# Optimization experiments

Measured on AMD Instinct MI355X. Metric: run time of the kernel, lower is better.

Reference implementation:

```python
import jax, jax.numpy as jnp
import numpy as np

B, S, L = 2, 512, 12
DIM, H, HD = 1024, 16, 64
MAX_SEQ, DFF = 1024, 4096
VOCAB, CODE_HEADS = 2048, 7
THETA, EPS = 10000.0, 1e-5


def _rope_tables():
    inv_freq = 1.0 / (THETA ** (jnp.arange(0, HD, 2, dtype=jnp.float32) / HD))
    t = jnp.arange(MAX_SEQ, dtype=jnp.float32)
    freqs = t[:, None] * inv_freq[None, :]          # [MAX, HD/2]
    emb = jnp.concatenate([freqs, freqs], axis=-1)  # [MAX, HD]
    return jnp.cos(emb), jnp.sin(emb)


def _rotate_half(x):
    x1, x2 = x[..., : HD // 2], x[..., HD // 2:]
    return jnp.concatenate([-x2, x1], axis=-1)


def _rms(x, w):
    v = jnp.mean(x * x, axis=-1, keepdims=True)
    return x * jax.lax.rsqrt(v + EPS) * w


def setup_inputs() -> dict:
    key = jax.random.key(0)
    ks = jax.random.split(key, 12)
    std = 0.02
    rn = lambda k, shp: jax.random.normal(k, shp, jnp.float32) * std
    fused_input2 = jax.random.normal(ks[0], (B, S, DIM), jnp.float32)
    primary_hidden = jax.random.normal(ks[1], (B, S, DIM), jnp.float32)
    position_ids = jnp.broadcast_to(jnp.arange(S), (B, S))
    cache_position = jnp.arange(S)
    # causal additive mask over the full cache length
    allowed = jnp.arange(MAX_SEQ)[None, :] <= cache_position[:, None]  # [S, MAX]
    attn_mask = jnp.broadcast_to(
        jnp.where(allowed, 0.0, -1e9)[None, None], (B, 1, S, MAX_SEQ)
    ).astype(jnp.float32)
    return {
        'fused_input2': fused_input2,
        'primary_hidden': primary_hidden,
        'attn_mask': attn_mask,
        'w_bridge': rn(ks[2], (2 * DIM, DIM)),
        'ln1_w': jnp.ones((L, DIM), jnp.float32),
        'wq': rn(ks[3], (L, DIM, DIM)),
        'wk': rn(ks[4], (L, DIM, DIM)),
        'wv': rn(ks[5], (L, DIM, DIM)),
        'wo': rn(ks[6], (L, DIM, DIM)),
        'ln2_w': jnp.ones((L, DIM), jnp.float32),
        'w_gate': rn(ks[7], (L, DIM, DFF)),
        'w_up': rn(ks[8], (L, DIM, DFF)),
        'w_down': rn(ks[9], (L, DFF, DIM)),
        'norm_w': jnp.ones((DIM,), jnp.float32),
        'w_out': rn(ks[10], (CODE_HEADS, DIM, VOCAB)),
        'position_ids': position_ids,
        'cache_position': cache_position,
    }


def reference(fused_input2, primary_hidden, attn_mask, w_bridge, ln1_w, wq, wk, wv,
              wo, ln2_w, w_gate, w_up, w_down, norm_w, w_out,
              position_ids, cache_position):
    rope_cos, rope_sin = _rope_tables()
    cos = rope_cos[position_ids][:, None]  # [B,1,S,HD]
    sin = rope_sin[position_ids][:, None]
    scale = 1.0 / np.sqrt(HD).astype(np.float32)
    h = jnp.concatenate([fused_input2, primary_hidden], axis=-1) @ w_bridge
    for i in range(L):
        x = _rms(h, ln1_w[i])
        q = (x @ wq[i]).reshape(B, S, H, HD).transpose(0, 2, 1, 3)
        k = (x @ wk[i]).reshape(B, S, H, HD).transpose(0, 2, 1, 3)
        v = (x @ wv[i]).reshape(B, S, H, HD).transpose(0, 2, 1, 3)
        q = q * cos + _rotate_half(q) * sin
        k = k * cos + _rotate_half(k) * sin
        # scatter-style KV-cache write at cache_position
        kc = jnp.zeros((B, H, MAX_SEQ, HD), x.dtype).at[:, :, cache_position, :].set(k)
        vc = jnp.zeros((B, H, MAX_SEQ, HD), x.dtype).at[:, :, cache_position, :].set(v)
        s = jnp.einsum('bhsd,bhtd->bhst', q, kc) * scale + attn_mask
        p = jax.nn.softmax(s.astype(jnp.float32), axis=-1).astype(x.dtype)
        o = jnp.einsum('bhst,bhtd->bhsd', p, vc).transpose(0, 2, 1, 3).reshape(B, S, DIM)
        h = h + o @ wo[i]
        r = h
        x = _rms(h, ln2_w[i])
        h = r + (jax.nn.silu(x @ w_gate[i]) * (x @ w_up[i])) @ w_down[i]
    h = _rms(h, norm_w)
    # [B, code_depth-1, S, VOCAB]
    return jnp.einsum('bsd,kdv->bksv', h, w_out).astype(jnp.float32)
```

## Files before the change

kernel.cpp:

```cpp
#include <hip/hip_runtime.h>

#define NB    2
#define SEQ   512
#define NL    12
#define DIM   1024
#define NH    16
#define HD    64
#define DFF   4096
#define VOCAB 2048
#define CHD   7

typedef __attribute__((ext_vector_type(4))) float f32x4;
typedef __attribute__((ext_vector_type(8))) short s16x8;
typedef __attribute__((ext_vector_type(4))) unsigned short u16x4;
typedef __attribute__((ext_vector_type(8))) unsigned short u16x8;

__device__ __forceinline__ unsigned short f2bf(float f) {
    unsigned u = __builtin_bit_cast(unsigned, f);
    u += 0x7fffu + ((u >> 16) & 1u);
    return (unsigned short)(u >> 16);
}

__device__ __forceinline__ void gl2lds16(const void* g, void* l) {
    __builtin_amdgcn_global_load_lds(
        (const __attribute__((address_space(1))) void*)g,
        (__attribute__((address_space(3))) void*)l, 16, 0, 0);
}

template<int EPI>
__global__ __launch_bounds__(256)
void gemm_bf(const unsigned short* __restrict__ A,
             const unsigned short* __restrict__ B0,
             const unsigned short* __restrict__ B1,
             const unsigned short* __restrict__ B2,
             float* __restrict__ C, int K, int lda, int ldbT, int ldc,
             int rhi, long sBz, long sCz, int kchunk, int ksplit,
             const float* __restrict__ tc, const float* __restrict__ ts,
             const int* __restrict__ pid, unsigned short* __restrict__ qkv_bf)
{
    __shared__ unsigned short sm[4][8192];

    const int tid = threadIdx.x;
    const int z   = blockIdx.z;
    const int wsel = z / ksplit, kz = z - wsel * ksplit;
    const int m0  = blockIdx.y * 128;
    const int n0  = blockIdx.x * 128;
    const int koff = kz * kchunk;

    const unsigned short* Ap = A + koff;
    const unsigned short* Bp = sBz ? (B0 + (long)wsel * sBz)
                                   : (wsel == 0 ? B0 : (wsel == 1 ? B1 : B2));
    Bp += koff;
    float* Cp = C + (long)wsel * sCz;

    const int w = tid >> 6, l = tid & 63;
    const int lrow = l & 15, lhi = l >> 4;
    const int wm = (w >> 1) * 64, wn = (w & 1) * 64;

    int rowS[4], colS[4];
    #pragma unroll
    for (int i = 0; i < 4; ++i) {
        const int c = w * 256 + i * 64 + l;
        rowS[i] = c >> 3;
        colS[i] = (((c & 7) ^ ((c >> 3) & 7)) << 3);
    }

    f32x4 acc[4][4] = {};

    auto STAGE = [&](int d, int k0) {
        unsigned short* Ab = &sm[d * 2][0];
        unsigned short* Bb = &sm[d * 2 + 1][0];
        #pragma unroll
        for (int i = 0; i < 4; ++i) {
            const int ub = (w * 256 + i * 64) * 8;
            gl2lds16(Ap + (long)(m0 + rowS[i]) * lda + k0 + colS[i], Ab + ub);
            gl2lds16(Bp + (long)(n0 + rowS[i]) * ldbT + k0 + colS[i], Bb + ub);
        }
    };
    auto COMPUTE = [&](int d) {
        const char* Ab = (const char*)&sm[d * 2][0];
        const char* Bb = (const char*)&sm[d * 2 + 1][0];
        #pragma unroll
        for (int ks = 0; ks < 2; ++ks) {
            s16x8 af[4], bf[4];
            #pragma unroll
            for (int i = 0; i < 4; ++i) {
                const int r = wm + i * 16 + lrow;
                af[i] = __builtin_bit_cast(s16x8, *reinterpret_cast<const u16x8*>(
                    Ab + r * 128 + (((ks * 4 + lhi) ^ (r & 7)) << 4)));
            }
            #pragma unroll
            for (int j = 0; j < 4; ++j) {
                const int r = wn + j * 16 + lrow;
                bf[j] = __builtin_bit_cast(s16x8, *reinterpret_cast<const u16x8*>(
                    Bb + r * 128 + (((ks * 4 + lhi) ^ (r & 7)) << 4)));
            }
            #pragma unroll
            for (int i = 0; i < 4; ++i)
                #pragma unroll
                for (int j = 0; j < 4; ++j)
                    acc[i][j] = __builtin_amdgcn_mfma_f32_16x16x32_bf16(af[i], bf[j], acc[i][j], 0, 0, 0);
        }
    };

    STAGE(0, 0);
    __syncthreads();
    int cur = 0;
    for (int k0 = 0; k0 < K; k0 += 64) {
        if (k0 + 64 < K) STAGE(cur ^ 1, k0 + 64);
        COMPUTE(cur);
        __syncthreads();
        cur ^= 1;
    }

    if (EPI == 2) {
        const int h = (n0 + wn) >> 6;
        unsigned short* qb = qkv_bf;
        unsigned short* kb = qkv_bf + 1048576;
        unsigned short* vt = qkv_bf + 2097152;
        #pragma unroll
        for (int i = 0; i < 4; ++i) {
            const int r0 = m0 + wm + i * 16 + lhi * 4;
            #pragma unroll
            for (int e = 0; e < 4; ++e) {
                const int r = r0 + e;
                if (wsel == 2) {
                    const int bh = (r >> 9) * NH + h, s = r & 511;
                    #pragma unroll
                    for (int j = 0; j < 4; ++j)
                        vt[((long)(bh * 64 + j * 16 + lrow)) * 512 + s] = f2bf(acc[i][j][e]);
                } else {
                    unsigned short* ob = (wsel == 0) ? qb : kb;
                    const int pos = pid[r];
                    const float c0 = tc[pos * 32 + lrow],      s0 = ts[pos * 32 + lrow];
                    const float c1 = tc[pos * 32 + 16 + lrow], s1 = ts[pos * 32 + 16 + lrow];
                    const float a0 = acc[i][0][e], a1 = acc[i][1][e];
                    const float a2 = acc[i][2][e], a3 = acc[i][3][e];
                    const long rb = (long)r * DIM + (n0 + wn) + lrow;
                    ob[rb]      = f2bf(a0 * c0 - a2 * s0);
                    ob[rb + 16] = f2bf(a1 * c1 - a3 * s1);
                    ob[rb + 32] = f2bf(a2 * c0 + a0 * s0);
                    ob[rb + 48] = f2bf(a3 * c1 + a1 * s1);
                }
            }
        }
        return;
    }

    #pragma unroll
    for (int i = 0; i < 4; ++i) {
        const int r0 = m0 + wm + i * 16 + lhi * 4;
        #pragma unroll
        for (int j = 0; j < 4; ++j) {
            const int c = n0 + wn + j * 16 + lrow;
            #pragma unroll
            for (int e = 0; e < 4; ++e) {
                const int r = r0 + e;
                const long idx = (long)(r >> 9) * rhi + (long)(r & 511) * ldc + c;
                if (EPI == 1) atomicAdd(&Cp[idx], acc[i][j][e]);
                else          Cp[idx] = acc[i][j][e];
            }
        }
    }
}

__global__ __launch_bounds__(256)
void gemm_gu(const unsigned short* __restrict__ A,
             const unsigned short* __restrict__ Bg0,
             const unsigned short* __restrict__ Bu0,
             unsigned short* __restrict__ GU, int K, int lda, int ldbT)
{
    __shared__ unsigned short sm[32768];
    char* const lds = (char*)sm;

    const int tid = threadIdx.x;
    const int m0  = blockIdx.y * 128;
    const int n0  = blockIdx.x * 64;

    const unsigned short* Bg = Bg0 + (long)n0 * ldbT;
    const unsigned short* Bu = Bu0 + (long)n0 * ldbT;

    const int w = tid >> 6, l = tid & 63;
    const int lrow = l & 15, lhi = l >> 4;
    const int wm = (w >> 1) * 64, wn = (w & 1) * 32;

    int rowA[4], colA[4];
    #pragma unroll
    for (int i = 0; i < 4; ++i) {
        const int c = w * 256 + i * 64 + l;
        rowA[i] = c >> 3;
        colA[i] = (((c & 7) ^ ((c >> 3) & 7)) << 3);
    }
    int rowB[2], colB[2];
    #pragma unroll
    for (int i = 0; i < 2; ++i) {
        const int c = w * 128 + i * 64 + l;
        rowB[i] = c >> 3;
        colB[i] = (((c & 7) ^ ((c >> 3) & 7)) << 3);
    }

    f32x4 accg[4][2] = {};
    f32x4 accu[4][2] = {};

    auto STAGE = [&](int d, int k0) {
        char* Ab  = lds + d * 16384;
        char* Bgb = lds + 32768 + d * 8192;
        char* Bub = lds + 49152 + d * 8192;
        #pragma unroll
        for (int i = 0; i < 4; ++i) {
            const int ub = (w * 256 + i * 64) * 16;
            gl2lds16(A + (long)(m0 + rowA[i]) * lda + k0 + colA[i], Ab + ub);
        }
        #pragma unroll
        for (int i = 0; i < 2; ++i) {
            const int ub = (w * 128 + i * 64) * 16;
            gl2lds16(Bg + (long)rowB[i] * ldbT + k0 + colB[i], Bgb + ub);
            gl2lds16(Bu + (long)rowB[i] * ldbT + k0 + colB[i], Bub + ub);
        }
    };
    auto COMPUTE = [&](int d) {
        const char* Ab  = lds + d * 16384;
        const char* Bgb = lds + 32768 + d * 8192;
        const char* Bub = lds + 49152 + d * 8192;
        #pragma unroll
        for (int ks = 0; ks < 2; ++ks) {
            s16x8 af[4], bg[2], bu[2];
            #pragma unroll
            for (int i = 0; i < 4; ++i) {
                const int r = wm + i * 16 + lrow;
                af[i] = __builtin_bit_cast(s16x8, *reinterpret_cast<const u16x8*>(
                    Ab + r * 128 + (((ks * 4 + lhi) ^ (r & 7)) << 4)));
            }
            #pragma unroll
            for (int j = 0; j < 2; ++j) {
                const int r = wn + j * 16 + lrow;
                const int off = r * 128 + (((ks * 4 + lhi) ^ (r & 7)) << 4);
                bg[j] = __builtin_bit_cast(s16x8, *reinterpret_cast<const u16x8*>(Bgb + off));
                bu[j] = __builtin_bit_cast(s16x8, *reinterpret_cast<const u16x8*>(Bub + off));
            }
            #pragma unroll
            for (int i = 0; i < 4; ++i)
                #pragma unroll
                for (int j = 0; j < 2; ++j) {
                    accg[i][j] = __builtin_amdgcn_mfma_f32_16x16x32_bf16(af[i], bg[j], accg[i][j], 0, 0, 0);
                    accu[i][j] = __builtin_amdgcn_mfma_f32_16x16x32_bf16(af[i], bu[j], accu[i][j], 0, 0, 0);
                }
        }
    };

    STAGE(0, 0);
    __syncthreads();
    int cur = 0;
    for (int k0 = 0; k0 < K; k0 += 64) {
        if (k0 + 64 < K) STAGE(cur ^ 1, k0 + 64);
        COMPUTE(cur);
        __syncthreads();
        cur ^= 1;
    }

    #pragma unroll
    for (int i = 0; i < 4; ++i) {
        const int r0 = m0 + wm + i * 16 + lhi * 4;
        #pragma unroll
        for (int j = 0; j < 2; ++j) {
            const int c = n0 + wn + j * 16 + lrow;
            #pragma unroll
            for (int e = 0; e < 4; ++e) {
                const float gx = accg[i][j][e];
                const float ux = accu[i][j][e];
                const float val = gx / (1.0f + __expf(-gx)) * ux;
                GU[(long)(r0 + e) * DFF + c] = f2bf(val);
            }
        }
    }
}

__global__ __launch_bounds__(256)
void tconv_kernel(const float* __restrict__ src, unsigned short* __restrict__ dst,
                  int R, int Cn, long sS, long sD)
{
    __shared__ float tile[64][65];
    const int c0 = blockIdx.x * 64, r0 = blockIdx.y * 64;
    const float* s = src + (long)blockIdx.z * sS;
    unsigned short* d = dst + (long)blockIdx.z * sD;
    const int tid = threadIdx.x;
    #pragma unroll
    for (int it = 0; it < 4; ++it) {
        const int idx = tid + it * 256;
        const int r = idx >> 4, c4 = (idx & 15) * 4;
        f32x4 v = *reinterpret_cast<const f32x4*>(&s[(long)(r0 + r) * Cn + c0 + c4]);
        tile[r][c4] = v[0]; tile[r][c4+1] = v[1]; tile[r][c4+2] = v[2]; tile[r][c4+3] = v[3];
    }
    __syncthreads();
    #pragma unroll
    for (int it = 0; it < 4; ++it) {
        const int idx = tid + it * 256;
        const int n = idx >> 4, r4 = (idx & 15) * 4;
        u16x4 o = { f2bf(tile[r4][n]), f2bf(tile[r4+1][n]),
                    f2bf(tile[r4+2][n]), f2bf(tile[r4+3][n]) };
        *reinterpret_cast<u16x4*>(&d[(long)(c0 + n) * R + r0 + r4]) = o;
    }
}

__global__ __launch_bounds__(256)
void ropetab_kernel(float* __restrict__ tc, float* __restrict__ ts)
{
    const int idx = blockIdx.x * 256 + threadIdx.x;
    const int pos = idx >> 5, i = idx & 31;
    const float invf = powf(10000.0f, -(float)i * (1.0f / 32.0f));
    const float ang = (float)pos * invf;
    tc[idx] = cosf(ang);
    ts[idx] = sinf(ang);
}

template<bool BF>
__global__ __launch_bounds__(256)
void concat_kernel(const float* __restrict__ a, const float* __restrict__ b,
                   void* __restrict__ outv)
{
    const long i = ((long)blockIdx.x * 256 + threadIdx.x) * 4;
    const int row = (int)(i >> 11), col = (int)(i & 2047);
    const float* src = (col < DIM) ? &a[(long)row * DIM + col]
                                   : &b[(long)row * DIM + col - DIM];
    f32x4 v = *reinterpret_cast<const f32x4*>(src);
    if (BF) {
        u16x4 o = { f2bf(v[0]), f2bf(v[1]), f2bf(v[2]), f2bf(v[3]) };
        *reinterpret_cast<u16x4*>((unsigned short*)outv + i) = o;
    } else {
        *reinterpret_cast<f32x4*>((float*)outv + i) = v;
    }
}

template<bool BF>
__global__ __launch_bounds__(256)
void rms_kernel(const float* __restrict__ in, const float* __restrict__ w,
                void* __restrict__ outv)
{
    __shared__ float red[4];
    const int row = blockIdx.x, tid = threadIdx.x;
    const long base = (long)row * DIM + tid * 4;
    f32x4 v = *reinterpret_cast<const f32x4*>(&in[base]);
    float ss = v[0]*v[0] + v[1]*v[1] + v[2]*v[2] + v[3]*v[3];
    for (int off = 32; off; off >>= 1) ss += __shfl_down(ss, off);
    if ((tid & 63) == 0) red[tid >> 6] = ss;
    __syncthreads();
    float s = red[0] + red[1] + red[2] + red[3];
    float r = 1.0f / sqrtf(s * (1.0f / DIM) + 1e-5f);
    f32x4 wv = *reinterpret_cast<const f32x4*>(&w[tid * 4]);
    f32x4 o = { v[0]*r*wv[0], v[1]*r*wv[1], v[2]*r*wv[2], v[3]*r*wv[3] };
    if (BF) {
        u16x4 ob = { f2bf(o[0]), f2bf(o[1]), f2bf(o[2]), f2bf(o[3]) };
        *reinterpret_cast<u16x4*>((unsigned short*)outv + base) = ob;
    } else {
        *reinterpret_cast<f32x4*>((float*)outv + base) = o;
    }
}

__global__ __launch_bounds__(256)
void attn_bf(const unsigned short* __restrict__ qb,
             const unsigned short* __restrict__ kb,
             const unsigned short* __restrict__ vt,
             unsigned short* __restrict__ attv)
{
    __shared__ unsigned short Qs[4096];
    __shared__ unsigned short Ps[64][72];
    __shared__ unsigned short Ks[2][4096];
    __shared__ unsigned short Vs[2][4096];
    const int tid = threadIdx.x;
    const int qt = blockIdx.x, bh = blockIdx.y, b = bh >> 4, h = bh & 15;
    const int q0 = qt * 64;
    const int w = tid >> 6, l = tid & 63, lrow = l & 15, lhi = l >> 4;

    int rowS[2], colS[2];
    #pragma unroll
    for (int i = 0; i < 2; ++i) {
        const int c = w * 128 + i * 64 + l;
        rowS[i] = c >> 3;
        colS[i] = (((c & 7) ^ ((c >> 3) & 7)) << 3);
    }

    auto STAGE64 = [&](const unsigned short* src, long rstride, unsigned short* dst) {
        #pragma unroll
        for (int i = 0; i < 2; ++i)
            gl2lds16(src + (long)rowS[i] * rstride + colS[i],
                     dst + (w * 128 + i * 64) * 8);
    };

    STAGE64(qb + (long)(b * SEQ + q0) * DIM + h * HD, DIM, Qs);

    auto STAGE_KV = [&](int kt, int d) {
        const int t0 = kt * 64;
        STAGE64(kb + (long)(b * SEQ + t0) * DIM + h * HD, DIM, Ks[d]);
        STAGE64(vt + (long)(bh * 64) * 512 + t0, 512, Vs[d]);
    };

    float m_run[4], l_run[4];
    f32x4 o[4] = {};
    #pragma unroll
    for (int j = 0; j < 4; ++j) { m_run[j] = -1e30f; l_run[j] = 0.f; }
    const float scale = 0.125f;

    STAGE_KV(0, 0);
    __syncthreads();

    for (int kt = 0; kt <= qt; ++kt) {
        const int cur = kt & 1;
        const int t0 = kt * 64;
        if (kt < qt) STAGE_KV(kt + 1, cur ^ 1);

        f32x4 s[4] = {};
        __builtin_amdgcn_s_setprio(1);
        #pragma unroll
        for (int ks = 0; ks < 2; ++ks) {
            const int rq = w * 16 + lrow;
            s16x8 aq = __builtin_bit_cast(s16x8, *reinterpret_cast<const u16x8*>(
                (const char*)Qs + rq * 128 + (((ks * 4 + lhi) ^ (rq & 7)) << 4)));
            #pragma unroll
            for (int j = 0; j < 4; ++j) {
                const int rk = j * 16 + lrow;
                s16x8 bk = __builtin_bit_cast(s16x8, *reinterpret_cast<const u16x8*>(
                    (const char*)Ks[cur] + rk * 128 + (((ks * 4 + lhi) ^ (rk & 7)) << 4)));
                s[j] = __builtin_amdgcn_mfma_f32_16x16x32_bf16(aq, bk, s[j], 0, 0, 0);
            }
        }
        __builtin_amdgcn_s_setprio(0);

        float pv[4][4], corr[4];
        #pragma unroll
        for (int j = 0; j < 4; ++j) {
            const int qrow = q0 + w * 16 + lhi * 4 + j;
            float sv[4], mx = -1e30f;
            #pragma unroll
            for (int tcq = 0; tcq < 4; ++tcq) {
                const int tcur = t0 + tcq * 16 + lrow;
                float vvv = s[tcq][j] * scale;
                if (tcur > qrow) vvv = -1e30f;
                sv[tcq] = vvv;
                mx = fmaxf(mx, vvv);
            }
            #pragma unroll
            for (int mk = 1; mk < 16; mk <<= 1) mx = fmaxf(mx, __shfl_xor(mx, mk));
            const float mnew = fmaxf(m_run[j], mx);
            const float c = __expf(m_run[j] - mnew);
            m_run[j] = mnew;
            float rs = 0.f;
            #pragma unroll
            for (int tcq = 0; tcq < 4; ++tcq) {
                float p = __expf(sv[tcq] - mnew);
                pv[tcq][j] = p;
                rs += p;
            }
            #pragma unroll
            for (int mk = 1; mk < 16; mk <<= 1) rs += __shfl_xor(rs, mk);
            l_run[j] = l_run[j] * c + rs;
            corr[j] = c;
        }

        #pragma unroll
        for (int tcq = 0; tcq < 4; ++tcq)
            #pragma unroll
            for (int j = 0; j < 4; ++j)
                Ps[w * 16 + lhi * 4 + j][tcq * 16 + lrow] = f2bf(pv[tcq][j]);

        #pragma unroll
        for (int dn = 0; dn < 4; ++dn)
            #pragma unroll
            for (int j = 0; j < 4; ++j)
                o[dn][j] *= corr[j];
        __builtin_amdgcn_s_setprio(1);
        #pragma unroll
        for (int ks = 0; ks < 2; ++ks) {
            s16x8 ap = __builtin_bit_cast(s16x8,
                *reinterpret_cast<const u16x8*>(&Ps[w * 16 + lrow][ks * 32 + lhi * 8]));
            #pragma unroll
            for (int dn = 0; dn < 4; ++dn) {
                const int rv = dn * 16 + lrow;
                s16x8 bv = __builtin_bit_cast(s16x8, *reinterpret_cast<const u16x8*>(
                    (const char*)Vs[cur] + rv * 128 + (((ks * 4 + lhi) ^ (rv & 7)) << 4)));
                o[dn] = __builtin_amdgcn_mfma_f32_16x16x32_bf16(ap, bv, o[dn], 0, 0, 0);
            }
        }
        __builtin_amdgcn_s_setprio(0);
        __syncthreads();
    }

    #pragma unroll
    for (int dn = 0; dn < 4; ++dn)
        #pragma unroll
        for (int j = 0; j < 4; ++j) {
            const int qrow = q0 + w * 16 + lhi * 4 + j;
            const int d = dn * 16 + lrow;
            const long idx = (((long)(b * SEQ + qrow)) * NH + h) * HD + d;
            attv[idx] = f2bf(o[dn][j] / l_run[j]);
        }
}

__device__ __forceinline__ int swz_b(int row, int col_u16) {
    return row * 128 + ((((col_u16 >> 3) ^ (row & 7)) << 4)) + ((col_u16 << 1) & 15);
}

template<bool ATOMIC, bool SILU>
__global__ __launch_bounds__(256)
void gemm128(const float* __restrict__ A, const float* __restrict__ A2,
             const float* __restrict__ B0, const float* __restrict__ B1,
             const float* __restrict__ B2, float* __restrict__ C,
             int K, int lda, int ldb, int ldc,
             int rhi, long sBz, long sCz, int kchunk)
{
    __shared__ unsigned short As[128 * 64];
    __shared__ unsigned short Bs[128 * 64];
    char* const Ab = reinterpret_cast<char*>(As);
    char* const Bb = reinterpret_cast<char*>(Bs);

    const int tid = threadIdx.x;
    const int z   = blockIdx.z;
    const int m0  = blockIdx.y * 128;
    const int n0  = blockIdx.x * 128;

    const float* Bp = sBz ? (B0 + (long)z * sBz) : (z == 0 ? B0 : (z == 1 ? B1 : B2));
    const long koff = (long)z * kchunk;
    const float* Ap  = A + koff;
    const float* A2p = SILU ? (A2 + koff) : nullptr;
    Bp += koff * (long)ldb;
    float* Cp = C + (long)z * sCz;

    const int w = tid >> 6, l = tid & 63;
    const int lrow = l & 15, lhi = l >> 4;
    const int wm = (w >> 1) * 64, wn = (w & 1) * 64;

    f32x4 acc[4][4] = {};

    for (int k0 = 0; k0 < K; k0 += 64) {
        __syncthreads();
        #pragma unroll
        for (int it = 0; it < 8; ++it) {
            const int idx = tid + it * 256;
            const int m = idx >> 4, c4 = (idx & 15) << 2;
            const long ga = (long)(m0 + m) * lda + k0 + c4;
            float4 v = *reinterpret_cast<const float4*>(&Ap[ga]);
            if (SILU) {
                const float4 v2 = *reinterpret_cast<const float4*>(&A2p[ga]);
                v.x = v.x / (1.0f + __expf(-v.x)) * v2.x;
                v.y = v.y / (1.0f + __expf(-v.y)) * v2.y;
                v.z = v.z / (1.0f + __expf(-v.z)) * v2.z;
                v.w = v.w / (1.0f + __expf(-v.w)) * v2.w;
            }
            u16x4 p = { f2bf(v.x), f2bf(v.y), f2bf(v.z), f2bf(v.w) };
            *reinterpret_cast<u16x4*>(Ab + swz_b(m, c4)) = p;
        }
        #pragma unroll
        for (int it = 0; it < 8; ++it) {
            const int idx = tid + it * 256;
            const int n = idx & 127, kq = idx >> 7;
            const long bb = (long)(k0 + kq * 4) * ldb + n0 + n;
            const float b0v = Bp[bb];
            const float b1v = Bp[bb + ldb];
            const float b2v = Bp[bb + 2 * (long)ldb];
            const float b3v = Bp[bb + 3 * (long)ldb];
            u16x4 p = { f2bf(b0v), f2bf(b1v), f2bf(b2v), f2bf(b3v) };
            *reinterpret_cast<u16x4*>(Bb + swz_b(n, kq << 2)) = p;
        }
        __syncthreads();

        #pragma unroll
        for (int ks = 0; ks < 2; ++ks) {
            s16x8 af[4], bfr[4];
            #pragma unroll
            for (int i = 0; i < 4; ++i) {
                const int r = wm + i * 16 + lrow;
                af[i] = __builtin_bit_cast(s16x8,
                    *reinterpret_cast<const u16x8*>(Ab + swz_b(r, ks * 32 + lhi * 8)));
            }
            #pragma unroll
            for (int j = 0; j < 4; ++j) {
                const int r = wn + j * 16 + lrow;
                bfr[j] = __builtin_bit_cast(s16x8,
                    *reinterpret_cast<const u16x8*>(Bb + swz_b(r, ks * 32 + lhi * 8)));
            }
            #pragma unroll
            for (int i = 0; i < 4; ++i)
                #pragma unroll
                for (int j = 0; j < 4; ++j)
                    acc[i][j] = __builtin_amdgcn_mfma_f32_16x16x32_bf16(af[i], bfr[j], acc[i][j], 0, 0, 0);
        }
    }

    #pragma unroll
    for (int i = 0; i < 4; ++i) {
        const int r0 = m0 + wm + i * 16 + lhi * 4;
        #pragma unroll
        for (int j = 0; j < 4; ++j) {
            const int c = n0 + wn + j * 16 + lrow;
            #pragma unroll
            for (int e = 0; e < 4; ++e) {
                const int r = r0 + e;
                const long idx = (long)(r >> 9) * rhi + (long)(r & 511) * ldc + c;
                if (ATOMIC) atomicAdd(&Cp[idx], acc[i][j][e]);
                else        Cp[idx] = acc[i][j][e];
            }
        }
    }
}

__global__ __launch_bounds__(256)
void rope_kernel(float* __restrict__ q, float* __restrict__ k,
                 const int* __restrict__ pid)
{
    const int t = blockIdx.x * 256 + threadIdx.x;
    const int i = t & 31, h = (t >> 5) & 15, s = (t >> 9) & 511, b = t >> 18;
    const int pos = pid[b * SEQ + s];
    const float invf = powf(10000.0f, -(float)i * (1.0f / 32.0f));
    const float ang = (float)pos * invf;
    const float c = cosf(ang), sn = sinf(ang);
    const long base = (((long)(b * SEQ + s)) * NH + h) * HD + i;
    float a1 = q[base], a2 = q[base + 32];
    q[base] = a1 * c - a2 * sn;  q[base + 32] = a2 * c + a1 * sn;
    float b1 = k[base], b2 = k[base + 32];
    k[base] = b1 * c - b2 * sn;  k[base + 32] = b2 * c + b1 * sn;
}

__global__ __launch_bounds__(256)
void transpose_v_kernel(const float* __restrict__ v, float* __restrict__ vT)
{
    __shared__ float tile[64][65];
    const int st = blockIdx.x, bh = blockIdx.y, b = bh >> 4, h = bh & 15;
    const int s0 = st * 64;
    for (int t = threadIdx.x; t < 64 * 16; t += 256) {
        int s = t >> 4, c4 = (t & 15) * 4;
        f32x4 v4 = *reinterpret_cast<const f32x4*>(
            &v[(((long)(b * SEQ + s0 + s)) * NH + h) * HD + c4]);
        tile[s][c4] = v4[0]; tile[s][c4+1] = v4[1]; tile[s][c4+2] = v4[2]; tile[s][c4+3] = v4[3];
    }
    __syncthreads();
    for (int t = threadIdx.x; t < 64 * 16; t += 256) {
        int d = t >> 4, c4 = (t & 15) * 4;
        f32x4 o4 = { tile[c4][d], tile[c4+1][d], tile[c4+2][d], tile[c4+3][d] };
        *reinterpret_cast<f32x4*>(&vT[((long)bh * HD + d) * SEQ + s0 + c4]) = o4;
    }
}

template<bool BF>
__global__ __launch_bounds__(256)
void attn_kernel(const float* __restrict__ q, const float* __restrict__ k,
                 const float* __restrict__ vT, void* __restrict__ attv)
{
    __shared__ unsigned short Qs[64][72];
    __shared__ unsigned short Ks[64][72];
    __shared__ unsigned short Ps[64][72];
    __shared__ unsigned short Vs[64][72];
    const int tid = threadIdx.x;
    const int qt = blockIdx.x, bh = blockIdx.y, b = bh >> 4, h = bh & 15;
    const int q0 = qt * 64;
    const int w = tid >> 6, l = tid & 63, lrow = l & 15, lhi = l >> 4;

    for (int t = tid; t < 64 * 16; t += 256) {
        int r = t >> 4, c4 = (t & 15) * 4;
        f32x4 v4 = *reinterpret_cast<const f32x4*>(
            &q[(((long)(b * SEQ + q0 + r)) * NH + h) * HD + c4]);
        u16x4 p = { f2bf(v4[0]), f2bf(v4[1]), f2bf(v4[2]), f2bf(v4[3]) };
        *reinterpret_cast<u16x4*>(&Qs[r][c4]) = p;
    }

    float m_run[4], l_run[4];
    f32x4 o[4] = {};
    #pragma unroll
    for (int j = 0; j < 4; ++j) { m_run[j] = -1e30f; l_run[j] = 0.f; }
    const float scale = 0.125f;

    for (int kt = 0; kt <= qt; ++kt) {
        const int t0 = kt * 64;
        __syncthreads();
        for (int t = tid; t < 64 * 16; t += 256) {
            int r = t >> 4, c4 = (t & 15) * 4;
            f32x4 v4 = *reinterpret_cast<const f32x4*>(
                &k[(((long)(b * SEQ + t0 + r)) * NH + h) * HD + c4]);
            u16x4 p = { f2bf(v4[0]), f2bf(v4[1]), f2bf(v4[2]), f2bf(v4[3]) };
            *reinterpret_cast<u16x4*>(&Ks[r][c4]) = p;
        }
        for (int t = tid; t < 64 * 16; t += 256) {
            int d = t >> 4, c4 = (t & 15) * 4;
            f32x4 v4 = *reinterpret_cast<const f32x4*>(
                &vT[((long)bh * HD + d) * SEQ + t0 + c4]);
            u16x4 p = { f2bf(v4[0]), f2bf(v4[1]), f2bf(v4[2]), f2bf(v4[3]) };
            *reinterpret_cast<u16x4*>(&Vs[d][c4]) = p;
        }
        __syncthreads();

        f32x4 s[4] = {};
        #pragma unroll
        for (int ks = 0; ks < 2; ++ks) {
            s16x8 aq = __builtin_bit_cast(s16x8,
                *reinterpret_cast<const u16x8*>(&Qs[w * 16 + lrow][ks * 32 + lhi * 8]));
            #pragma unroll
            for (int j = 0; j < 4; ++j) {
                s16x8 bk = __builtin_bit_cast(s16x8,
                    *reinterpret_cast<const u16x8*>(&Ks[j * 16 + lrow][ks * 32 + lhi * 8]));
                s[j] = __builtin_amdgcn_mfma_f32_16x16x32_bf16(aq, bk, s[j], 0, 0, 0);
            }
        }

        float pv[4][4], corr[4];
        #pragma unroll
        for (int j = 0; j < 4; ++j) {
            const int qrow = q0 + w * 16 + lhi * 4 + j;
            float sv[4], mx = -1e30f;
            #pragma unroll
            for (int tcq = 0; tcq < 4; ++tcq) {
                const int tcur = t0 + tcq * 16 + lrow;
                float vvv = s[tcq][j] * scale;
                if (tcur > qrow) vvv = -1e30f;
                sv[tcq] = vvv;
                mx = fmaxf(mx, vvv);
            }
            #pragma unroll
            for (int mk = 1; mk < 16; mk <<= 1) mx = fmaxf(mx, __shfl_xor(mx, mk));
            const float mnew = fmaxf(m_run[j], mx);
            const float c = __expf(m_run[j] - mnew);
            m_run[j] = mnew;
            float rs = 0.f;
            #pragma unroll
            for (int tcq = 0; tcq < 4; ++tcq) {
                float p = __expf(sv[tcq] - mnew);
                pv[tcq][j] = p;
                rs += p;
            }
            #pragma unroll
            for (int mk = 1; mk < 16; mk <<= 1) rs += __shfl_xor(rs, mk);
            l_run[j] = l_run[j] * c + rs;
            corr[j] = c;
        }

        #pragma unroll
        for (int tcq = 0; tcq < 4; ++tcq)
            #pragma unroll
            for (int j = 0; j < 4; ++j)
                Ps[w * 16 + lhi * 4 + j][tcq * 16 + lrow] = f2bf(pv[tcq][j]);

        #pragma unroll
        for (int dn = 0; dn < 4; ++dn)
            #pragma unroll
            for (int j = 0; j < 4; ++j)
                o[dn][j] *= corr[j];
        #pragma unroll
        for (int ks = 0; ks < 2; ++ks) {
            s16x8 ap = __builtin_bit_cast(s16x8,
                *reinterpret_cast<const u16x8*>(&Ps[w * 16 + lrow][ks * 32 + lhi * 8]));
            #pragma unroll
            for (int dn = 0; dn < 4; ++dn) {
                s16x8 bv = __builtin_bit_cast(s16x8,
                    *reinterpret_cast<const u16x8*>(&Vs[dn * 16 + lrow][ks * 32 + lhi * 8]));
                o[dn] = __builtin_amdgcn_mfma_f32_16x16x32_bf16(ap, bv, o[dn], 0, 0, 0);
            }
        }
    }

    #pragma unroll
    for (int dn = 0; dn < 4; ++dn)
        #pragma unroll
        for (int j = 0; j < 4; ++j) {
            const int qrow = q0 + w * 16 + lhi * 4 + j;
            const int d = dn * 16 + lrow;
            const long idx = (((long)(b * SEQ + qrow)) * NH + h) * HD + d;
            const float val = o[dn][j] / l_run[j];
            if (BF) ((unsigned short*)attv)[idx] = f2bf(val);
            else    ((float*)attv)[idx] = val;
        }
}

__global__ __launch_bounds__(256)
void silu_bf_kernel(const float* __restrict__ g, const float* __restrict__ u,
                    unsigned short* __restrict__ o)
{
    const long i = ((long)blockIdx.x * 256 + threadIdx.x) * 4;
    f32x4 gv = *reinterpret_cast<const f32x4*>(&g[i]);
    f32x4 uv = *reinterpret_cast<const f32x4*>(&u[i]);
    u16x4 r;
    #pragma unroll
    for (int e = 0; e < 4; ++e) {
        float gx = gv[e];
        r[e] = f2bf(gx / (1.0f + __expf(-gx)) * uv[e]);
    }
    *reinterpret_cast<u16x4*>(&o[i]) = r;
}

extern "C" void kernel_launch(void* const* d_in, const int* in_sizes, int n_in,
                              void* d_out, int out_size, void* d_ws, size_t ws_size,
                              hipStream_t stream)
{
    const float* f2   = (const float*)d_in[0];
    const float* ph   = (const float*)d_in[1];
    const float* wbr  = (const float*)d_in[3];
    const float* ln1  = (const float*)d_in[4];
    const float* wq   = (const float*)d_in[5];
    const float* wk   = (const float*)d_in[6];
    const float* wv   = (const float*)d_in[7];
    const float* wo   = (const float*)d_in[8];
    const float* ln2  = (const float*)d_in[9];
    const float* wg   = (const float*)d_in[10];
    const float* wu   = (const float*)d_in[11];
    const float* wd   = (const float*)d_in[12];
    const float* nw   = (const float*)d_in[13];
    const float* wout = (const float*)d_in[14];
    const int*   pid  = (const int*)d_in[15];
    float* out = (float*)d_out;

    const long M1 = 1048576;
    dim3 blk(256);

    const size_t NEED = (size_t)122 * M1 * 4;
    if (ws_size >= NEED) {
        float* ws = (float*)d_ws;
        float* h    = ws;
        float* tcos = ws + 1 * M1;
        float* tsin = ws + 1 * M1 + 16384;
        unsigned short* xcat_bf = (unsigned short*)(ws + 2 * M1);
        unsigned short* x_bf    = (unsigned short*)(ws + 3 * M1);
        unsigned short* att_bf  = (unsigned short*)(ws + 3 * M1 + 524288);
        unsigned short* gu_bf   = (unsigned short*)(ws + 4 * M1);
        unsigned short* qkv_bf  = (unsigned short*)(ws + 6 * M1);
        unsigned short* wT      = (unsigned short*)(ws + 17 * M1);
        unsigned short* wbrT  = wT;
        unsigned short* wqT   = wbrT + 2 * M1;
        unsigned short* wkT   = wqT + 12 * M1;
        unsigned short* wvT   = wkT + 12 * M1;
        unsigned short* woT   = wvT + 12 * M1;
        unsigned short* wgT   = woT + 12 * M1;
        unsigned short* wuT   = wgT + 48 * M1;
        unsigned short* wdT   = wuT + 48 * M1;
        unsigned short* woutT = wdT + 48 * M1;

        ropetab_kernel<<<64, blk, 0, stream>>>(tcos, tsin);
        tconv_kernel<<<dim3(16, 32, 1), blk, 0, stream>>>(wbr, wbrT, 2048, 1024, 0, 0);
        tconv_kernel<<<dim3(16, 16, NL), blk, 0, stream>>>(wq, wqT, 1024, 1024, M1, M1);
        tconv_kernel<<<dim3(16, 16, NL), blk, 0, stream>>>(wk, wkT, 1024, 1024, M1, M1);
        tconv_kernel<<<dim3(16, 16, NL), blk, 0, stream>>>(wv, wvT, 1024, 1024, M1, M1);
        tconv_kernel<<<dim3(16, 16, NL), blk, 0, stream>>>(wo, woT, 1024, 1024, M1, M1);
        tconv_kernel<<<dim3(64, 16, NL), blk, 0, stream>>>(wg, wgT, 1024, 4096, 4 * M1, 4 * M1);
        tconv_kernel<<<dim3(64, 16, NL), blk, 0, stream>>>(wu, wuT, 1024, 4096, 4 * M1, 4 * M1);
        tconv_kernel<<<dim3(16, 64, NL), blk, 0, stream>>>(wd, wdT, 4096, 1024, 4 * M1, 4 * M1);
        tconv_kernel<<<dim3(32, 16, CHD), blk, 0, stream>>>(wout, woutT, 1024, 2048, 2 * M1, 2 * M1);

        concat_kernel<true><<<2048, blk, 0, stream>>>(f2, ph, xcat_bf);
        hipMemsetAsync(h, 0, M1 * 4, stream);
        gemm_bf<1><<<dim3(8, 8, 4), blk, 0, stream>>>(
            xcat_bf, wbrT, wbrT, wbrT, h, 512, 2048, 2048, 1024, 512 * 1024, 0, 0, 512, 4,
            nullptr, nullptr, nullptr, nullptr);

        for (int i = 0; i < NL; ++i) {
            rms_kernel<true><<<1024, blk, 0, stream>>>(h, ln1 + (long)i * DIM, x_bf);
            gemm_bf<2><<<dim3(8, 8, 3), blk, 0, stream>>>(
                x_bf, wqT + (long)i * M1, wkT + (long)i * M1, wvT + (long)i * M1, nullptr,
                1024, 1024, 1024, 1024, 0, 0, 0, 0, 1,
                tcos, tsin, pid, qkv_bf);
            attn_bf<<<dim3(8, 32), blk, 0, stream>>>(
                qkv_bf, qkv_bf + M1, qkv_bf + 2 * M1, att_bf);
            gemm_bf<1><<<dim3(8, 8, 4), blk, 0, stream>>>(
                att_bf, woT + (long)i * M1, woT + (long)i * M1, woT + (long)i * M1, h,
                256, 1024, 1024, 1024, 512 * 1024, 0, 0, 256, 4,
                nullptr, nullptr, nullptr, nullptr);

            rms_kernel<true><<<1024, blk, 0, stream>>>(h, ln2 + (long)i * DIM, x_bf);
            gemm_gu<<<dim3(64, 8), blk, 0, stream>>>(
                x_bf, wgT + (long)i * 4 * M1, wuT + (long)i * 4 * M1, gu_bf, 1024, 1024, 1024);
            gemm_bf<1><<<dim3(8, 8, 8), blk, 0, stream>>>(
                gu_bf, wdT + (long)i * 4 * M1, wdT + (long)i * 4 * M1, wdT + (long)i * 4 * M1, h,
                512, 4096, 4096, 1024, 512 * 1024, 0, 0, 512, 8,
                nullptr, nullptr, nullptr, nullptr);
        }

        rms_kernel<true><<<1024, blk, 0, stream>>>(h, nw, x_bf);
        gemm_bf<0><<<dim3(16, 8, CHD), blk, 0, stream>>>(
            x_bf, woutT, nullptr, nullptr, out,
            1024, 1024, 1024, 2048, CHD * 512 * 2048, 2 * M1, (long)512 * 2048, 0, 1,
            nullptr, nullptr, nullptr, nullptr);
        return;
    }

    float* ws = (float*)d_ws;
    float* xcat = ws;
    float* h    = ws + 2 * M1;
    float* x    = ws + 3 * M1;
    float* q    = ws + 4 * M1;
    float* kb   = ws + 5 * M1;
    float* v    = ws + 6 * M1;
    float* vT   = ws + 7 * M1;
    float* att  = ws + 8 * M1;
    float* g    = ws + 9 * M1;
    float* u    = ws + 13 * M1;

    concat_kernel<false><<<2048, blk, 0, stream>>>(f2, ph, xcat);
    gemm128<false, false><<<dim3(8, 8, 1), blk, 0, stream>>>(
        xcat, nullptr, wbr, wbr, wbr, h, 2048, 2048, DIM, DIM, 512 * DIM, 0, 0, 0);

    for (int i = 0; i < NL; ++i) {
        rms_kernel<false><<<1024, blk, 0, stream>>>(h, ln1 + (long)i * DIM, x);
        gemm128<false, false><<<dim3(8, 8, 3), blk, 0, stream>>>(
            x, nullptr, wq + (long)i * M1, wk + (long)i * M1, wv + (long)i * M1, q,
            1024, DIM, DIM, DIM, 512 * DIM, 0, M1, 0);
        rope_kernel<<<2048, blk, 0, stream>>>(q, kb, pid);
        transpose_v_kernel<<<dim3(8, 32), blk, 0, stream>>>(v, vT);
        attn_kernel<false><<<dim3(8, 32), blk, 0, stream>>>(q, kb, vT, att);
        gemm128<true, false><<<dim3(8, 8, 2), blk, 0, stream>>>(
            att, nullptr, wo + (long)i * M1, wo + (long)i * M1, wo + (long)i * M1, h,
            512, DIM, DIM, DIM, 512 * DIM, 0, 0, 512);

        rms_kernel<false><<<1024, blk, 0, stream>>>(h, ln2 + (long)i * DIM, x);
        gemm128<false, false><<<dim3(32, 8, 1), blk, 0, stream>>>(
            x, nullptr, wg + (long)i * 4 * M1, wg + (long)i * 4 * M1, wg + (long)i * 4 * M1, g,
            1024, DIM, DFF, DFF, 512 * DFF, 0, 0, 0);
        gemm128<false, false><<<dim3(32, 8, 1), blk, 0, stream>>>(
            x, nullptr, wu + (long)i * 4 * M1, wu + (long)i * 4 * M1, wu + (long)i * 4 * M1, u,
            1024, DIM, DFF, DFF, 512 * DFF, 0, 0, 0);
        gemm128<true, true><<<dim3(8, 8, 4), blk, 0, stream>>>(
            g, u, wd + (long)i * 4 * M1, wd + (long)i * 4 * M1, wd + (long)i * 4 * M1, h,
            1024, DFF, DIM, DIM, 512 * DIM, 0, 0, 1024);
    }

    rms_kernel<false><<<1024, blk, 0, stream>>>(h, nw, x);
    gemm128<false, false><<<dim3(16, 8, CHD), blk, 0, stream>>>(
        x, nullptr, wout, wout, wout, out,
        1024, DIM, VOCAB, VOCAB, CHD * 512 * VOCAB, (long)DIM * VOCAB, (long)512 * VOCAB, 0);
}
```

Before: 1.847 ms.

## Drop LDS double-buffering in GEMMs and double split-K for atomic GEMMs

Replaces the double-buffered LDS prefetch pipeline in gemm_bf and gemm_gu with a single buffer: each K step now does sync, load, sync, compute. This halves the LDS footprint per block, which can let more blocks share a CU. The split-K factor for the bridge, output-projection and down-projection GEMMs is also doubled, giving more blocks for the 256-CU device but twice as many float atomic adds into h. It gives up overlap between global loads and MFMA inside a block and adds a barrier per K step, relying on more resident blocks to hide latency.

```diff
diff --git a/kernel.cpp b/kernel.cpp
--- a/kernel.cpp
+++ b/kernel.cpp
@@ -38,7 +38,7 @@
              const float* __restrict__ tc, const float* __restrict__ ts,
              const int* __restrict__ pid, unsigned short* __restrict__ qkv_bf)
 {
-    __shared__ unsigned short sm[4][8192];
+    __shared__ unsigned short sm[2][8192];
 
     const int tid = threadIdx.x;
     const int z   = blockIdx.z;
@@ -67,9 +67,9 @@
 
     f32x4 acc[4][4] = {};
 
-    auto STAGE = [&](int d, int k0) {
-        unsigned short* Ab = &sm[d * 2][0];
-        unsigned short* Bb = &sm[d * 2 + 1][0];
+    auto STAGE = [&](int k0) {
+        unsigned short* Ab = &sm[0][0];
+        unsigned short* Bb = &sm[1][0];
         #pragma unroll
         for (int i = 0; i < 4; ++i) {
             const int ub = (w * 256 + i * 64) * 8;
@@ -77,9 +77,9 @@
             gl2lds16(Bp + (long)(n0 + rowS[i]) * ldbT + k0 + colS[i], Bb + ub);
         }
     };
-    auto COMPUTE = [&](int d) {
-        const char* Ab = (const char*)&sm[d * 2][0];
-        const char* Bb = (const char*)&sm[d * 2 + 1][0];
+    auto COMPUTE = [&]() {
+        const char* Ab = (const char*)&sm[0][0];
+        const char* Bb = (const char*)&sm[1][0];
         #pragma unroll
         for (int ks = 0; ks < 2; ++ks) {
             s16x8 af[4], bf[4];
@@ -103,14 +103,11 @@
         }
     };
 
-    STAGE(0, 0);
-    __syncthreads();
-    int cur = 0;
     for (int k0 = 0; k0 < K; k0 += 64) {
-        if (k0 + 64 < K) STAGE(cur ^ 1, k0 + 64);
-        COMPUTE(cur);
+        if (k0) __syncthreads();
+        STAGE(k0);
         __syncthreads();
-        cur ^= 1;
+        COMPUTE();
     }
 
     if (EPI == 2) {
@@ -170,7 +167,7 @@
              const unsigned short* __restrict__ Bu0,
              unsigned short* __restrict__ GU, int K, int lda, int ldbT)
 {
-    __shared__ unsigned short sm[32768];
+    __shared__ unsigned short sm[16384];
     char* const lds = (char*)sm;
 
     const int tid = threadIdx.x;
@@ -202,10 +199,10 @@
     f32x4 accg[4][2] = {};
     f32x4 accu[4][2] = {};
 
-    auto STAGE = [&](int d, int k0) {
-        char* Ab  = lds + d * 16384;
-        char* Bgb = lds + 32768 + d * 8192;
-        char* Bub = lds + 49152 + d * 8192;
+    auto STAGE = [&](int k0) {
+        char* Ab  = lds;
+        char* Bgb = lds + 16384;
+        char* Bub = lds + 24576;
         #pragma unroll
         for (int i = 0; i < 4; ++i) {
             const int ub = (w * 256 + i * 64) * 16;
@@ -218,10 +215,10 @@
             gl2lds16(Bu + (long)rowB[i] * ldbT + k0 + colB[i], Bub + ub);
         }
     };
-    auto COMPUTE = [&](int d) {
-        const char* Ab  = lds + d * 16384;
-        const char* Bgb = lds + 32768 + d * 8192;
-        const char* Bub = lds + 49152 + d * 8192;
+    auto COMPUTE = [&]() {
+        const char* Ab  = lds;
+        const char* Bgb = lds + 16384;
+        const char* Bub = lds + 24576;
         #pragma unroll
         for (int ks = 0; ks < 2; ++ks) {
             s16x8 af[4], bg[2], bu[2];
@@ -248,14 +245,11 @@
         }
     };
 
-    STAGE(0, 0);
-    __syncthreads();
-    int cur = 0;
     for (int k0 = 0; k0 < K; k0 += 64) {
-        if (k0 + 64 < K) STAGE(cur ^ 1, k0 + 64);
-        COMPUTE(cur);
+        if (k0) __syncthreads();
+        STAGE(k0);
         __syncthreads();
-        cur ^= 1;
+        COMPUTE();
     }
 
     #pragma unroll
@@ -842,8 +836,8 @@
 
         concat_kernel<true><<<2048, blk, 0, stream>>>(f2, ph, xcat_bf);
         hipMemsetAsync(h, 0, M1 * 4, stream);
-        gemm_bf<1><<<dim3(8, 8, 4), blk, 0, stream>>>(
-            xcat_bf, wbrT, wbrT, wbrT, h, 512, 2048, 2048, 1024, 512 * 1024, 0, 0, 512, 4,
+        gemm_bf<1><<<dim3(8, 8, 8), blk, 0, stream>>>(
+            xcat_bf, wbrT, wbrT, wbrT, h, 256, 2048, 2048, 1024, 512 * 1024, 0, 0, 256, 8,
             nullptr, nullptr, nullptr, nullptr);
 
         for (int i = 0; i < NL; ++i) {
@@ -854,17 +848,17 @@
                 tcos, tsin, pid, qkv_bf);
             attn_bf<<<dim3(8, 32), blk, 0, stream>>>(
                 qkv_bf, qkv_bf + M1, qkv_bf + 2 * M1, att_bf);
-            gemm_bf<1><<<dim3(8, 8, 4), blk, 0, stream>>>(
+            gemm_bf<1><<<dim3(8, 8, 8), blk, 0, stream>>>(
                 att_bf, woT + (long)i * M1, woT + (long)i * M1, woT + (long)i * M1, h,
-                256, 1024, 1024, 1024, 512 * 1024, 0, 0, 256, 4,
+                128, 1024, 1024, 1024, 512 * 1024, 0, 0, 128, 8,
                 nullptr, nullptr, nullptr, nullptr);
 
             rms_kernel<true><<<1024, blk, 0, stream>>>(h, ln2 + (long)i * DIM, x_bf);
             gemm_gu<<<dim3(64, 8), blk, 0, stream>>>(
                 x_bf, wgT + (long)i * 4 * M1, wuT + (long)i * 4 * M1, gu_bf, 1024, 1024, 1024);
-            gemm_bf<1><<<dim3(8, 8, 8), blk, 0, stream>>>(
+            gemm_bf<1><<<dim3(8, 8, 16), blk, 0, stream>>>(
                 gu_bf, wdT + (long)i * 4 * M1, wdT + (long)i * 4 * M1, wdT + (long)i * 4 * M1, h,
-                512, 4096, 4096, 1024, 512 * 1024, 0, 0, 512, 8,
+                256, 4096, 4096, 1024, 512 * 1024, 0, 0, 256, 16,
                 nullptr, nullptr, nullptr, nullptr);
         }
 
```

Measured after the change: 2.361 ms. +27.8%, slower.
